# Performance work log

Hardware: AMD Instinct MI355X
Metric: run time of the kernel (lower is better)

The kernel has to match this reference:

```python
import jax, jax.numpy as jnp
import numpy as np

N, D, M = 262144, 64, 256
CLAMP = -1e-9  # clamp_max value for the ray denominator


def setup_inputs() -> dict:
    key = jax.random.key(0)
    kz, kp, ka, kb = jax.random.split(key, 4)
    return {
        "z": jax.random.normal(kz, (N, D), dtype=jnp.float32),
        "pivot": jax.random.normal(kp, (D,), dtype=jnp.float32),
        "At": jax.random.normal(ka, (D, M), dtype=jnp.float32),
        "b": jax.random.normal(kb, (M,), dtype=jnp.float32),
    }


def reference(z, pivot, At, b):
    # sign_arg: [N, M] — signed constraint violation A z - b
    sign_arg = z @ At - b[None, :]
    ind = sign_arg >= 0  # violated constraints
    ray = pivot[None, :] - z  # [N, D] direction toward the interior pivot
    # denominator clamped to <= -1e-9 and detached (constant w.r.t. grads)
    denom = jax.lax.stop_gradient(jnp.minimum(ray @ At, CLAMP))  # [N, M]
    alpha = -sign_arg / denom
    # step size = max over violated constraints (alpha*ind zeros out satisfied ones)
    common_alpha = jnp.max(alpha * ind.astype(alpha.dtype), axis=1)  # [N]
    common_ind = jnp.any(ind, axis=1)  # [N] — move only if some constraint violated
    return z + common_ind[:, None].astype(z.dtype) * (common_alpha[:, None] * ray)
```

## Files before the change

kernel.cpp:

```cpp
#include <hip/hip_runtime.h>

#define DIMK 64
#define MC 256
#define BR 64
#define NROWS 262144
#define NB (NROWS / BR)

#define WS_AT 1024
#define WS_NEED (1024 + 65536)

#define LDS_AH 0
#define LDS_AL 16384
#define LDS_GM 32768
#define LDS_ZT 0
#define LDS_GM2 16384

typedef _Float16 half8 __attribute__((ext_vector_type(8)));
typedef float f32x16 __attribute__((ext_vector_type(16)));

__global__ void precompute_c(const float* __restrict__ pivot,
                             const float* __restrict__ At,
                             float* __restrict__ ws) {
    const int t = threadIdx.x;
    float acc = 0.f;
#pragma unroll
    for (int k = 0; k < DIMK; ++k) acc = fmaf(pivot[k], At[k * MC + t], acc);
    ws[t] = acc;
}

__global__ void precompute_at(const float* __restrict__ pivot,
                              const float* __restrict__ At,
                              float* __restrict__ ws) {
    const int t = threadIdx.x;
    float col[DIMK];
    float acc = 0.f;
#pragma unroll
    for (int k = 0; k < DIMK; ++k) {
        col[k] = At[k * MC + t];
        acc = fmaf(pivot[k], col[k], acc);
    }
    ws[t] = acc;
    char* wsb = (char*)ws + WS_AT;
#pragma unroll
    for (int s = 0; s < 2; ++s) {
#pragma unroll
        for (int kc = 0; kc < 4; ++kc) {
            half8 h, l;
#pragma unroll
            for (int j = 0; j < 8; ++j) {
                const float v = col[s * 32 + kc * 8 + j];
                h[j] = (_Float16)v;
                l[j] = (_Float16)(v - (float)h[j]);
            }
            const int off = ((s * 4 + kc) * 256 + t) * 16;
            *(half8*)(wsb + off) = h;
            *(half8*)(wsb + off + 32768) = l;
        }
    }
}

template <bool PREAT>
__global__ __launch_bounds__(256, 4)
void fused_constrain_mfma(const float* __restrict__ z,
                          const float* __restrict__ pivot,
                          const float* __restrict__ At,
                          const float* __restrict__ b,
                          const float* __restrict__ ws,
                          float* __restrict__ out) {
    __shared__ __align__(16) char lds[33280];

    const int tid  = threadIdx.x;
    const int lane = tid & 63;
    const int li   = lane & 31;
    const int hi   = lane >> 5;
    const int wid  = tid >> 6;
    const int rg   = wid >> 1;
    const int cg   = wid & 1;
    const int R0   = rg * 32;
    const int colbase = cg * 128;
    const int base = blockIdx.x * (BR * DIMK);

    float4 zf[8];
    {
        const float* zr = z + base + (R0 + li) * DIMK + hi * 8;
#pragma unroll
        for (int q = 0; q < 4; ++q) {
            const float* p = zr + (q >> 1) * 32 + (q & 1) * 16;
            zf[q * 2 + 0] = *(const float4*)(p);
            zf[q * 2 + 1] = *(const float4*)(p + 4);
        }
    }

    if constexpr (PREAT) {
        const int zrow = R0 + li;
        const int rx = zrow & 15;
        char* zt = lds + LDS_ZT + zrow * 256;
#pragma unroll
        for (int q = 0; q < 4; ++q) {
            const int c0 = hi * 2 + (q >> 1) * 8 + (q & 1) * 4;
            *(float4*)(zt + ((c0 ^ rx) << 4))       = zf[q * 2 + 0];
            *(float4*)(zt + (((c0 + 1) ^ rx) << 4)) = zf[q * 2 + 1];
        }
    } else {
        const int swzT = (tid & 3) ^ ((tid >> 2) & 3);
#pragma unroll
        for (int kc = 0; kc < 4; ++kc) {
            float v[8];
#pragma unroll
            for (int j = 0; j < 8; ++j)
                v[j] = At[(kc * 8 + j) * MC + tid];
            half8 h, l;
#pragma unroll
            for (int j = 0; j < 8; ++j) {
                h[j] = (_Float16)v[j];
                l[j] = (_Float16)(v[j] - (float)h[j]);
            }
            const int off = tid * 64 + ((kc ^ swzT) << 4);
            *(half8*)(lds + LDS_AH + off) = h;
            *(half8*)(lds + LDS_AL + off) = l;
        }
    }

    half8 azh[4], azl[4];
    const float* zv = (const float*)zf;
#pragma unroll
    for (int q = 0; q < 4; ++q)
#pragma unroll
        for (int j = 0; j < 8; ++j) {
            const float v = zv[q * 8 + j];
            azh[q][j] = (_Float16)v;
            azl[q][j] = (_Float16)(v - (float)azh[q][j]);
        }

    f32x16 acc[4];
#pragma unroll
    for (int ct = 0; ct < 4; ++ct)
#pragma unroll
        for (int e = 0; e < 16; ++e) acc[ct][e] = 0.f;

    if constexpr (PREAT) {
        const char* pb = (const char*)ws + WS_AT + (hi * 256 + colbase + li) * 16;
#pragma unroll
        for (int s = 0; s < 2; ++s)
#pragma unroll
            for (int ksl = 0; ksl < 2; ++ksl) {
                const half8 ah = azh[s * 2 + ksl], al = azl[s * 2 + ksl];
                const int ob = s * 16384 + ksl * 8192;
#pragma unroll
                for (int ct = 0; ct < 4; ++ct) {
                    const half8 bh = *(const half8*)(pb + ob + ct * 512);
                    const half8 bl = *(const half8*)(pb + ob + ct * 512 + 32768);
                    acc[ct] = __builtin_amdgcn_mfma_f32_32x32x16_f16(ah, bh, acc[ct], 0, 0, 0);
                    acc[ct] = __builtin_amdgcn_mfma_f32_32x32x16_f16(ah, bl, acc[ct], 0, 0, 0);
                    acc[ct] = __builtin_amdgcn_mfma_f32_32x32x16_f16(al, bh, acc[ct], 0, 0, 0);
                }
            }
    } else {
        const int swz = (li & 3) ^ ((li >> 2) & 3);
        __syncthreads();
#pragma unroll
        for (int ksl = 0; ksl < 2; ++ksl) {
            const int cb = ((ksl * 2 + hi) ^ swz) << 4;
            const half8 ah = azh[ksl], al = azl[ksl];
#pragma unroll
            for (int ct = 0; ct < 4; ++ct) {
                const int off = (colbase + ct * 32 + li) * 64 + cb;
                const half8 bh = *(const half8*)(lds + LDS_AH + off);
                const half8 bl = *(const half8*)(lds + LDS_AL + off);
                acc[ct] = __builtin_amdgcn_mfma_f32_32x32x16_f16(ah, bh, acc[ct], 0, 0, 0);
                acc[ct] = __builtin_amdgcn_mfma_f32_32x32x16_f16(ah, bl, acc[ct], 0, 0, 0);
                acc[ct] = __builtin_amdgcn_mfma_f32_32x32x16_f16(al, bh, acc[ct], 0, 0, 0);
            }
        }
        __syncthreads();
        const int swzT = (tid & 3) ^ ((tid >> 2) & 3);
#pragma unroll
        for (int kc = 0; kc < 4; ++kc) {
            float v[8];
#pragma unroll
            for (int j = 0; j < 8; ++j)
                v[j] = At[(32 + kc * 8 + j) * MC + tid];
            half8 h, l;
#pragma unroll
            for (int j = 0; j < 8; ++j) {
                h[j] = (_Float16)v[j];
                l[j] = (_Float16)(v[j] - (float)h[j]);
            }
            const int off = tid * 64 + ((kc ^ swzT) << 4);
            *(half8*)(lds + LDS_AH + off) = h;
            *(half8*)(lds + LDS_AL + off) = l;
        }
        __syncthreads();
#pragma unroll
        for (int ksl = 0; ksl < 2; ++ksl) {
            const int cb = ((ksl * 2 + hi) ^ swz) << 4;
            const half8 ah = azh[2 + ksl], al = azl[2 + ksl];
#pragma unroll
            for (int ct = 0; ct < 4; ++ct) {
                const int off = (colbase + ct * 32 + li) * 64 + cb;
                const half8 bh = *(const half8*)(lds + LDS_AH + off);
                const half8 bl = *(const half8*)(lds + LDS_AL + off);
                acc[ct] = __builtin_amdgcn_mfma_f32_32x32x16_f16(ah, bh, acc[ct], 0, 0, 0);
                acc[ct] = __builtin_amdgcn_mfma_f32_32x32x16_f16(ah, bl, acc[ct], 0, 0, 0);
                acc[ct] = __builtin_amdgcn_mfma_f32_32x32x16_f16(al, bh, acc[ct], 0, 0, 0);
            }
        }
    }

    float bv[4], cv[4];
#pragma unroll
    for (int ct = 0; ct < 4; ++ct) {
        const int c = colbase + ct * 32 + li;
        bv[ct] = b[c];
        cv[ct] = ws[c];
    }
    float gm[16];
#pragma unroll
    for (int r = 0; r < 16; ++r) gm[r] = 0.f;
#pragma unroll
    for (int ct = 0; ct < 4; ++ct)
#pragma unroll
        for (int r = 0; r < 16; ++r) {
            const float sv = acc[ct][r];
            const float sa = sv - bv[ct];
            const float qd = fmaxf(sv - cv[ct], 1e-9f);
            gm[r] = fmaxf(gm[r], sa * __builtin_amdgcn_rcpf(qd));
        }
#pragma unroll
    for (int r = 0; r < 16; ++r)
#pragma unroll
        for (int off = 1; off < 32; off <<= 1)
            gm[r] = fmaxf(gm[r], __shfl_xor(gm[r], off));

    float* gmbuf = (float*)(lds + (PREAT ? LDS_GM2 : LDS_GM));
#pragma unroll
    for (int r = 0; r < 16; ++r) {
        const int row = (r & 3) + 8 * (r >> 2) + 4 * hi;
        if (li == 0) gmbuf[rg * 64 + row * 2 + cg] = gm[r];
    }
    __syncthreads();

    const float2 p2 = *(const float2*)(pivot + 2 * li);
    const int r0 = cg * 8;
#pragma unroll
    for (int rr = 0; rr < 8; ++rr) {
        const int r   = r0 + rr;
        const int row = (r & 3) + 8 * (r >> 2) + 4 * hi;
        const float g = fmaxf(gm[r], gmbuf[rg * 64 + row * 2 + (cg ^ 1)]);
        const int zrow = R0 + row;
        float2 zz;
        if constexpr (PREAT) {
            const int byt = LDS_ZT + zrow * 256 +
                            (((li >> 1) ^ (zrow & 15)) << 4) + (li & 1) * 8;
            zz = *(const float2*)(lds + byt);
        } else {
            zz = *(const float2*)(z + base + zrow * DIMK + 2 * li);
        }
        float2 o;
        o.x = fmaf(g, p2.x - zz.x, zz.x);
        o.y = fmaf(g, p2.y - zz.y, zz.y);
        *(float2*)(out + base + zrow * DIMK + 2 * li) = o;
    }
}

extern "C" void kernel_launch(void* const* d_in, const int* in_sizes, int n_in,
                              void* d_out, int out_size, void* d_ws, size_t ws_size,
                              hipStream_t stream) {
    const float* z     = (const float*)d_in[0];
    const float* pivot = (const float*)d_in[1];
    const float* At    = (const float*)d_in[2];
    const float* b     = (const float*)d_in[3];
    float* ws = (float*)d_ws;
    if (ws_size >= (size_t)WS_NEED) {
        precompute_at<<<dim3(1), dim3(MC), 0, stream>>>(pivot, At, ws);
        fused_constrain_mfma<true><<<dim3(NB), dim3(256), 0, stream>>>(
            z, pivot, At, b, ws, (float*)d_out);
    } else {
        precompute_c<<<dim3(1), dim3(MC), 0, stream>>>(pivot, At, ws);
        fused_constrain_mfma<false><<<dim3(NB), dim3(256), 0, stream>>>(
            z, pivot, At, b, ws, (float*)d_out);
    }
}
```

Measured before the change: 161.4 us.

## Make fused kernel persistent with LDS-resident At and double-buffered z prefetch

```diff
diff --git a/kernel.cpp b/kernel.cpp
--- a/kernel.cpp
+++ b/kernel.cpp
@@ -4,7 +4,9 @@
 #define MC 256
 #define BR 64
 #define NROWS 262144
-#define NB (NROWS / BR)
+#define NT (NROWS / BR)
+#define PB 512
+#define TPB (NT / PB)
 
 #define WS_AT 1024
 #define WS_NEED (1024 + 65536)
@@ -12,8 +14,9 @@
 #define LDS_AH 0
 #define LDS_AL 16384
 #define LDS_GM 32768
-#define LDS_ZT 0
-#define LDS_GM2 16384
+#define LDS_FB_SIZE 33280
+#define LDS_GM3 65536
+#define LDS_FP_SIZE 66560
 
 typedef _Float16 half8 __attribute__((ext_vector_type(8)));
 typedef float f32x16 __attribute__((ext_vector_type(16)));
@@ -60,14 +63,14 @@
 }
 
 template <bool PREAT>
-__global__ __launch_bounds__(256, 4)
+__global__ __launch_bounds__(256, 2)
 void fused_constrain_mfma(const float* __restrict__ z,
                           const float* __restrict__ pivot,
                           const float* __restrict__ At,
                           const float* __restrict__ b,
                           const float* __restrict__ ws,
                           float* __restrict__ out) {
-    __shared__ __align__(16) char lds[33280];
+    extern __shared__ __align__(16) char lds[];
 
     const int tid  = threadIdx.x;
     const int lane = tid & 63;
@@ -78,37 +81,153 @@
     const int cg   = wid & 1;
     const int R0   = rg * 32;
     const int colbase = cg * 128;
-    const int base = blockIdx.x * (BR * DIMK);
-
-    float4 zf[8];
-    {
-        const float* zr = z + base + (R0 + li) * DIMK + hi * 8;
-#pragma unroll
-        for (int q = 0; q < 4; ++q) {
-            const float* p = zr + (q >> 1) * 32 + (q & 1) * 16;
-            zf[q * 2 + 0] = *(const float4*)(p);
-            zf[q * 2 + 1] = *(const float4*)(p + 4);
-        }
-    }
 
     if constexpr (PREAT) {
-        const int zrow = R0 + li;
-        const int rx = zrow & 15;
-        char* zt = lds + LDS_ZT + zrow * 256;
-#pragma unroll
-        for (int q = 0; q < 4; ++q) {
-            const int c0 = hi * 2 + (q >> 1) * 8 + (q & 1) * 4;
-            *(float4*)(zt + ((c0 ^ rx) << 4))       = zf[q * 2 + 0];
-            *(float4*)(zt + (((c0 + 1) ^ rx) << 4)) = zf[q * 2 + 1];
+        float bv[4], cv[4];
+#pragma unroll
+        for (int ct = 0; ct < 4; ++ct) {
+            const int c = colbase + ct * 32 + li;
+            bv[ct] = b[c];
+            cv[ct] = ws[c];
+        }
+        const float2 p2 = *(const float2*)(pivot + 2 * li);
+
+        float4 zfA[8], zfB[8];
+        {
+            const float* zr = z + blockIdx.x * (TPB * BR * DIMK) +
+                              (R0 + li) * DIMK + hi * 8;
+#pragma unroll
+            for (int q = 0; q < 4; ++q) {
+                const float* p = zr + (q >> 1) * 32 + (q & 1) * 16;
+                zfA[q * 2 + 0] = *(const float4*)(p);
+                zfA[q * 2 + 1] = *(const float4*)(p + 4);
+            }
+        }
+
+        {
+            const char* wsA = (const char*)ws + WS_AT;
+#pragma unroll
+            for (int p = 0; p < 16; ++p) {
+                const int f = p * 256 + tid;
+                *(float4*)(lds + f * 16) = *(const float4*)(wsA + f * 16);
+            }
+        }
+        __syncthreads();
+
+        const int Boff = hi * 4096 + (colbase + li) * 16;
+
+        auto tile_body = [&](float4 (&zc)[8], float4 (&zn)[8],
+                             const int i, const bool pf) {
+            const int tbase = (blockIdx.x * TPB + i) * (BR * DIMK);
+
+            if (pf) {
+                const float* zr = z + tbase + BR * DIMK +
+                                  (R0 + li) * DIMK + hi * 8;
+#pragma unroll
+                for (int q = 0; q < 4; ++q) {
+                    const float* p = zr + (q >> 1) * 32 + (q & 1) * 16;
+                    zn[q * 2 + 0] = *(const float4*)(p);
+                    zn[q * 2 + 1] = *(const float4*)(p + 4);
+                }
+            }
+
+            half8 azh[4], azl[4];
+            const float* zv = (const float*)zc;
+#pragma unroll
+            for (int q = 0; q < 4; ++q)
+#pragma unroll
+                for (int j = 0; j < 8; ++j) {
+                    const float v = zv[q * 8 + j];
+                    azh[q][j] = (_Float16)v;
+                    azl[q][j] = (_Float16)(v - (float)azh[q][j]);
+                }
+
+            f32x16 acc[4];
+#pragma unroll
+            for (int ct = 0; ct < 4; ++ct)
+#pragma unroll
+                for (int e = 0; e < 16; ++e) acc[ct][e] = 0.f;
+
+#pragma unroll
+            for (int s = 0; s < 2; ++s)
+#pragma unroll
+                for (int ksl = 0; ksl < 2; ++ksl) {
+                    const half8 ah = azh[s * 2 + ksl], al = azl[s * 2 + ksl];
+                    const int ob = Boff + s * 16384 + ksl * 8192;
+#pragma unroll
+                    for (int ct = 0; ct < 4; ++ct) {
+                        const half8 bh = *(const half8*)(lds + ob + ct * 512);
+                        const half8 bl = *(const half8*)(lds + ob + ct * 512 + 32768);
+                        acc[ct] = __builtin_amdgcn_mfma_f32_32x32x16_f16(ah, bh, acc[ct], 0, 0, 0);
+                        acc[ct] = __builtin_amdgcn_mfma_f32_32x32x16_f16(ah, bl, acc[ct], 0, 0, 0);
+                        acc[ct] = __builtin_amdgcn_mfma_f32_32x32x16_f16(al, bh, acc[ct], 0, 0, 0);
+                    }
+                }
+
+            float gm[16];
+#pragma unroll
+            for (int r = 0; r < 16; ++r) gm[r] = 0.f;
+#pragma unroll
+            for (int ct = 0; ct < 4; ++ct)
+#pragma unroll
+                for (int r = 0; r < 16; ++r) {
+                    const float sv = acc[ct][r];
+                    const float sa = sv - bv[ct];
+                    const float qd = fmaxf(sv - cv[ct], 1e-9f);
+                    gm[r] = fmaxf(gm[r], sa * __builtin_amdgcn_rcpf(qd));
+                }
+#pragma unroll
+            for (int r = 0; r < 16; ++r)
+#pragma unroll
+                for (int off = 1; off < 32; off <<= 1)
+                    gm[r] = fmaxf(gm[r], __shfl_xor(gm[r], off));
+
+            float* gmb = (float*)(lds + LDS_GM3 + ((i & 1) << 9));
+#pragma unroll
+            for (int r = 0; r < 16; ++r) {
+                const int row = (r & 3) + 8 * (r >> 2) + 4 * hi;
+                if (li == 0) gmb[rg * 64 + row * 2 + cg] = gm[r];
+            }
+            __syncthreads();
+
+            const int r0 = cg * 8;
+#pragma unroll
+            for (int rr = 0; rr < 8; ++rr) {
+                const int r   = r0 + rr;
+                const int row = (r & 3) + 8 * (r >> 2) + 4 * hi;
+                const float g = fmaxf(gm[r], gmb[rg * 64 + row * 2 + (cg ^ 1)]);
+                const int idx = tbase + (R0 + row) * DIMK + 2 * li;
+                const float2 zz = *(const float2*)(z + idx);
+                float2 o;
+                o.x = fmaf(g, p2.x - zz.x, zz.x);
+                o.y = fmaf(g, p2.y - zz.y, zz.y);
+                *(float2*)(out + idx) = o;
+            }
+        };
+
+#pragma clang loop unroll(disable)
+        for (int j = 0; j < TPB / 2; ++j) {
+            tile_body(zfA, zfB, 2 * j, true);
+            tile_body(zfB, zfA, 2 * j + 1, j < TPB / 2 - 1);
         }
     } else {
+        const int base = blockIdx.x * (BR * DIMK);
+        float4 zf[8];
+        {
+            const float* zr = z + base + (R0 + li) * DIMK + hi * 8;
+#pragma unroll
+            for (int q = 0; q < 4; ++q) {
+                const float* p = zr + (q >> 1) * 32 + (q & 1) * 16;
+                zf[q * 2 + 0] = *(const float4*)(p);
+                zf[q * 2 + 1] = *(const float4*)(p + 4);
+            }
+        }
         const int swzT = (tid & 3) ^ ((tid >> 2) & 3);
 #pragma unroll
         for (int kc = 0; kc < 4; ++kc) {
             float v[8];
 #pragma unroll
-            for (int j = 0; j < 8; ++j)
-                v[j] = At[(kc * 8 + j) * MC + tid];
+            for (int j = 0; j < 8; ++j) v[j] = At[(kc * 8 + j) * MC + tid];
             half8 h, l;
 #pragma unroll
             for (int j = 0; j < 8; ++j) {
@@ -119,43 +238,24 @@
             *(half8*)(lds + LDS_AH + off) = h;
             *(half8*)(lds + LDS_AL + off) = l;
         }
-    }
-
-    half8 azh[4], azl[4];
-    const float* zv = (const float*)zf;
-#pragma unroll
-    for (int q = 0; q < 4; ++q)
-#pragma unroll
-        for (int j = 0; j < 8; ++j) {
-            const float v = zv[q * 8 + j];
-            azh[q][j] = (_Float16)v;
-            azl[q][j] = (_Float16)(v - (float)azh[q][j]);
-        }
-
-    f32x16 acc[4];
-#pragma unroll
-    for (int ct = 0; ct < 4; ++ct)
-#pragma unroll
-        for (int e = 0; e < 16; ++e) acc[ct][e] = 0.f;
-
-    if constexpr (PREAT) {
-        const char* pb = (const char*)ws + WS_AT + (hi * 256 + colbase + li) * 16;
-#pragma unroll
-        for (int s = 0; s < 2; ++s)
-#pragma unroll
-            for (int ksl = 0; ksl < 2; ++ksl) {
-                const half8 ah = azh[s * 2 + ksl], al = azl[s * 2 + ksl];
-                const int ob = s * 16384 + ksl * 8192;
-#pragma unroll
-                for (int ct = 0; ct < 4; ++ct) {
-                    const half8 bh = *(const half8*)(pb + ob + ct * 512);
-                    const half8 bl = *(const half8*)(pb + ob + ct * 512 + 32768);
-                    acc[ct] = __builtin_amdgcn_mfma_f32_32x32x16_f16(ah, bh, acc[ct], 0, 0, 0);
-                    acc[ct] = __builtin_amdgcn_mfma_f32_32x32x16_f16(ah, bl, acc[ct], 0, 0, 0);
-                    acc[ct] = __builtin_amdgcn_mfma_f32_32x32x16_f16(al, bh, acc[ct], 0, 0, 0);
-                }
-            }
-    } else {
+
+        half8 azh[4], azl[4];
+        const float* zv = (const float*)zf;
+#pragma unroll
+        for (int q = 0; q < 4; ++q)
+#pragma unroll
+            for (int j = 0; j < 8; ++j) {
+                const float v = zv[q * 8 + j];
+                azh[q][j] = (_Float16)v;
+                azl[q][j] = (_Float16)(v - (float)azh[q][j]);
+            }
+
+        f32x16 acc[4];
+#pragma unroll
+        for (int ct = 0; ct < 4; ++ct)
+#pragma unroll
+            for (int e = 0; e < 16; ++e) acc[ct][e] = 0.f;
+
         const int swz = (li & 3) ^ ((li >> 2) & 3);
         __syncthreads();
 #pragma unroll
@@ -173,13 +273,11 @@
             }
         }
         __syncthreads();
-        const int swzT = (tid & 3) ^ ((tid >> 2) & 3);
 #pragma unroll
         for (int kc = 0; kc < 4; ++kc) {
             float v[8];
 #pragma unroll
-            for (int j = 0; j < 8; ++j)
-                v[j] = At[(32 + kc * 8 + j) * MC + tid];
+            for (int j = 0; j < 8; ++j) v[j] = At[(32 + kc * 8 + j) * MC + tid];
             half8 h, l;
 #pragma unroll
             for (int j = 0; j < 8; ++j) {
@@ -205,61 +303,54 @@
                 acc[ct] = __builtin_amdgcn_mfma_f32_32x32x16_f16(al, bh, acc[ct], 0, 0, 0);
             }
         }
-    }
-
-    float bv[4], cv[4];
-#pragma unroll
-    for (int ct = 0; ct < 4; ++ct) {
-        const int c = colbase + ct * 32 + li;
-        bv[ct] = b[c];
-        cv[ct] = ws[c];
-    }
-    float gm[16];
-#pragma unroll
-    for (int r = 0; r < 16; ++r) gm[r] = 0.f;
-#pragma unroll
-    for (int ct = 0; ct < 4; ++ct)
+
+        float bv[4], cv[4];
+#pragma unroll
+        for (int ct = 0; ct < 4; ++ct) {
+            const int c = colbase + ct * 32 + li;
+            bv[ct] = b[c];
+            cv[ct] = ws[c];
+        }
+        float gm[16];
+#pragma unroll
+        for (int r = 0; r < 16; ++r) gm[r] = 0.f;
+#pragma unroll
+        for (int ct = 0; ct < 4; ++ct)
+#pragma unroll
+            for (int r = 0; r < 16; ++r) {
+                const float sv = acc[ct][r];
+                const float sa = sv - bv[ct];
+                const float qd = fmaxf(sv - cv[ct], 1e-9f);
+                gm[r] = fmaxf(gm[r], sa * __builtin_amdgcn_rcpf(qd));
+            }
+#pragma unroll
+        for (int r = 0; r < 16; ++r)
+#pragma unroll
+            for (int off = 1; off < 32; off <<= 1)
+                gm[r] = fmaxf(gm[r], __shfl_xor(gm[r], off));
+
+        float* gmbuf = (float*)(lds + LDS_GM);
 #pragma unroll
         for (int r = 0; r < 16; ++r) {
-            const float sv = acc[ct][r];
-            const float sa = sv - bv[ct];
-            const float qd = fmaxf(sv - cv[ct], 1e-9f);
-            gm[r] = fmaxf(gm[r], sa * __builtin_amdgcn_rcpf(qd));
-        }
-#pragma unroll
-    for (int r = 0; r < 16; ++r)
-#pragma unroll
-        for (int off = 1; off < 32; off <<= 1)
-            gm[r] = fmaxf(gm[r], __shfl_xor(gm[r], off));
-
-    float* gmbuf = (float*)(lds + (PREAT ? LDS_GM2 : LDS_GM));
-#pragma unroll
-    for (int r = 0; r < 16; ++r) {
-        const int row = (r & 3) + 8 * (r >> 2) + 4 * hi;
-        if (li == 0) gmbuf[rg * 64 + row * 2 + cg] = gm[r];
-    }
-    __syncthreads();
-
-    const float2 p2 = *(const float2*)(pivot + 2 * li);
-    const int r0 = cg * 8;
-#pragma unroll
-    for (int rr = 0; rr < 8; ++rr) {
-        const int r   = r0 + rr;
-        const int row = (r & 3) + 8 * (r >> 2) + 4 * hi;
-        const float g = fmaxf(gm[r], gmbuf[rg * 64 + row * 2 + (cg ^ 1)]);
-        const int zrow = R0 + row;
-        float2 zz;
-        if constexpr (PREAT) {
-            const int byt = LDS_ZT + zrow * 256 +
-                            (((li >> 1) ^ (zrow & 15)) << 4) + (li & 1) * 8;
-            zz = *(const float2*)(lds + byt);
-        } else {
-            zz = *(const float2*)(z + base + zrow * DIMK + 2 * li);
-        }
-        float2 o;
-        o.x = fmaf(g, p2.x - zz.x, zz.x);
-        o.y = fmaf(g, p2.y - zz.y, zz.y);
-        *(float2*)(out + base + zrow * DIMK + 2 * li) = o;
+            const int row = (r & 3) + 8 * (r >> 2) + 4 * hi;
+            if (li == 0) gmbuf[rg * 64 + row * 2 + cg] = gm[r];
+        }
+        __syncthreads();
+
+        const float2 p2 = *(const float2*)(pivot + 2 * li);
+        const int r0 = cg * 8;
+#pragma unroll
+        for (int rr = 0; rr < 8; ++rr) {
+            const int r   = r0 + rr;
+            const int row = (r & 3) + 8 * (r >> 2) + 4 * hi;
+            const float g = fmaxf(gm[r], gmbuf[rg * 64 + row * 2 + (cg ^ 1)]);
+            const int idx = base + (R0 + row) * DIMK + 2 * li;
+            const float2 zz = *(const float2*)(z + idx);
+            float2 o;
+            o.x = fmaf(g, p2.x - zz.x, zz.x);
+            o.y = fmaf(g, p2.y - zz.y, zz.y);
+            *(float2*)(out + idx) = o;
+        }
     }
 }
 
@@ -273,11 +364,11 @@
     float* ws = (float*)d_ws;
     if (ws_size >= (size_t)WS_NEED) {
         precompute_at<<<dim3(1), dim3(MC), 0, stream>>>(pivot, At, ws);
-        fused_constrain_mfma<true><<<dim3(NB), dim3(256), 0, stream>>>(
+        fused_constrain_mfma<true><<<dim3(PB), dim3(256), LDS_FP_SIZE, stream>>>(
             z, pivot, At, b, ws, (float*)d_out);
     } else {
         precompute_c<<<dim3(1), dim3(MC), 0, stream>>>(pivot, At, ws);
-        fused_constrain_mfma<false><<<dim3(NB), dim3(256), 0, stream>>>(
+        fused_constrain_mfma<false><<<dim3(NT), dim3(256), LDS_FB_SIZE, stream>>>(
             z, pivot, At, b, ws, (float*)d_out);
     }
 }
```

Result: faster. 156.9 us (-2.8%).
